# Optimization experiments

Hardware: AMD Instinct MI355X
Metric: run time of the kernel (lower is better)

The kernel has to match this reference:

```python
import jax, jax.numpy as jnp
import numpy as np
import math

B, S, D, H = 2, 2048, 1024, 16
DK = D // H


def setup_inputs() -> dict:
    key = jax.random.key(0)
    ks = jax.random.split(key, 8)
    s = 1.0 / math.sqrt(D)
    inp = {
        "query": jax.random.normal(ks[0], (B, S, D), jnp.float32),
        "key": jax.random.normal(ks[1], (B, S, D), jnp.float32),
        "value": jax.random.normal(ks[2], (B, S, D), jnp.float32),
        # causal mask: (1, 1, S, S), 1 where attention allowed
        "mask": jnp.tril(jnp.ones((S, S), jnp.int32))[None, None, :, :],
        "Wq": jax.random.normal(ks[3], (D, D), jnp.float32) * s,
        "Wk": jax.random.normal(ks[4], (D, D), jnp.float32) * s,
        "Wv": jax.random.normal(ks[5], (D, D), jnp.float32) * s,
        "Wo": jax.random.normal(ks[6], (D, D), jnp.float32) * s,
    }
    return inp


def reference(query, key, value, mask, Wq, Wk, Wv, Wo):
    # nn.Linear(bias=False): y = x @ W.T
    def proj_heads(x, W):
        y = jnp.einsum("bsd,ed->bse", x, W)          # (B,S,D)
        return y.reshape(B, -1, H, DK).transpose(0, 2, 1, 3)  # (B,H,S,DK)

    q = proj_heads(query, Wq)
    k = proj_heads(key, Wk)
    v = proj_heads(value, Wv)

    scale = jnp.asarray(math.sqrt(DK), q.dtype)
    scores = jnp.einsum("bhqd,bhkd->bhqk", q, k) / scale  # (B,H,S,S)
    scores = jnp.where(mask == 0, -jnp.inf, scores)
    attn = jax.nn.softmax(scores, axis=-1)
    # dropout p=0.0 (eval): identity
    out = jnp.einsum("bhqk,bhkd->bhqd", attn, v)          # (B,H,S,DK)
    concat = out.transpose(0, 2, 1, 3).reshape(B, -1, D)  # (B,S,D)
    return jnp.einsum("bsd,ed->bse", concat, Wo)
```

## Files before the change

### kernel.cpp

```cpp
#include <hip/hip_runtime.h>
#include <hip/hip_bf16.h>

#define B_ 2
#define S_ 2048
#define D_ 1024
#define H_ 16
#define DK_ 64

typedef __hip_bfloat16 bf16;
typedef __attribute__((ext_vector_type(8))) short bf16x8;
typedef __attribute__((ext_vector_type(4))) short bf16x4;
typedef __attribute__((ext_vector_type(4))) float f32x4;

#define GLDS16(g, l)                                                     \
    __builtin_amdgcn_global_load_lds(                                    \
        (const __attribute__((address_space(1))) void*)(g),              \
        (__attribute__((address_space(3))) void*)(l), 16, 0, 0)

#define MFMA_K32(a, b, c) __builtin_amdgcn_mfma_f32_16x16x32_bf16(a, b, c, 0, 0, 0)
#define MFMA_K16(a, b, c) __builtin_amdgcn_mfma_f32_16x16x16bf16_1k(a, b, c, 0, 0, 0)
#define EXP2F(x) __builtin_amdgcn_exp2f(x)

__global__ __launch_bounds__(256) void cvt_all(
    const float* __restrict__ q, const float* __restrict__ k, const float* __restrict__ v,
    const float* __restrict__ w0, const float* __restrict__ w1,
    const float* __restrict__ w2, const float* __restrict__ w3,
    bf16* __restrict__ oq, bf16* __restrict__ ok, bf16* __restrict__ ov,
    bf16* __restrict__ o0, bf16* __restrict__ o1, bf16* __restrict__ o2,
    bf16* __restrict__ o3) {
    int bid = blockIdx.x;
    const float* src; bf16* dst; int base;
    if      (bid < 2048) { src = q;  dst = oq; base = bid; }
    else if (bid < 4096) { src = k;  dst = ok; base = bid - 2048; }
    else if (bid < 6144) { src = v;  dst = ov; base = bid - 4096; }
    else if (bid < 6656) { src = w0; dst = o0; base = bid - 6144; }
    else if (bid < 7168) { src = w1; dst = o1; base = bid - 6656; }
    else if (bid < 7680) { src = w2; dst = o2; base = bid - 7168; }
    else                 { src = w3; dst = o3; base = bid - 7680; }
    int i = (base * 256 + threadIdx.x) * 8;
    float4 a = *(const float4*)(src + i);
    float4 b = *(const float4*)(src + i + 4);
    __align__(16) bf16 o[8];
    o[0] = __float2bfloat16(a.x); o[1] = __float2bfloat16(a.y);
    o[2] = __float2bfloat16(a.z); o[3] = __float2bfloat16(a.w);
    o[4] = __float2bfloat16(b.x); o[5] = __float2bfloat16(b.y);
    o[6] = __float2bfloat16(b.z); o[7] = __float2bfloat16(b.w);
    *(bf16x8*)(dst + i) = *(const bf16x8*)o;
}

template <int NT>
__device__ __forceinline__ void proj_loop(const bf16* __restrict__ X,
                                          const bf16* __restrict__ W,
                                          int m0, int n0, bf16* As, bf16* Bs,
                                          f32x4 (&acc)[2][NT]) {
    const int K = D_;
    const int tid = threadIdx.x;
    const int lane = tid & 63, wave = tid >> 6;
    const int lm = lane & 15, quad = lane >> 4;
    constexpr int BROWS = NT * 16;

    auto stage = [&](int t, int bf) {
        int k0 = t * 32;
        bf16* Ab = As + bf * (128 * 32);
        bf16* Bb = Bs + bf * (BROWS * 32);
#pragma unroll
        for (int i = 0; i < 2; ++i) {
            int s = i * 256 + tid;
            int row = s >> 2;
            int c = (s & 3) ^ ((row >> 1) & 3);
            GLDS16(X + (size_t)(m0 + row) * K + k0 + c * 8, Ab + s * 8);
        }
#pragma unroll
        for (int i = 0; i < NT / 4; ++i) {
            int s = i * 256 + tid;
            int row = s >> 2;
            int c = (s & 3) ^ ((row >> 1) & 3);
            GLDS16(W + (size_t)(n0 + row) * K + k0 + c * 8, Bb + s * 8);
        }
    };

    stage(0, 0);
    for (int t = 0; t < K / 32; ++t) {
        __syncthreads();
        if (t + 1 < K / 32) stage(t + 1, (t + 1) & 1);
        const bf16* Ab = As + (t & 1) * (128 * 32);
        const bf16* Bb = Bs + (t & 1) * (BROWS * 32);
        bf16x8 aF[2], bF[NT];
#pragma unroll
        for (int mt = 0; mt < 2; ++mt) {
            int row = wave * 32 + mt * 16 + lm;
            aF[mt] = *(const bf16x8*)(Ab + row * 32 + (quad ^ ((row >> 1) & 3)) * 8);
        }
#pragma unroll
        for (int nt = 0; nt < NT; ++nt) {
            int row = nt * 16 + lm;
            bF[nt] = *(const bf16x8*)(Bb + row * 32 + (quad ^ ((row >> 1) & 3)) * 8);
        }
#pragma unroll
        for (int mt = 0; mt < 2; ++mt)
#pragma unroll
            for (int nt = 0; nt < NT; ++nt)
                acc[mt][nt] = MFMA_K32(aF[mt], bF[nt], acc[mt][nt]);
    }
}

__global__ __launch_bounds__(256) void proj_qkv(
    const bf16* __restrict__ qx, const bf16* __restrict__ kx, const bf16* __restrict__ vx,
    const bf16* __restrict__ wq, const bf16* __restrict__ wk, const bf16* __restrict__ wv,
    bf16* __restrict__ qb, bf16* __restrict__ kb, bf16* __restrict__ vtb) {
    __shared__ __align__(16) bf16 As[2 * 128 * 32];
    __shared__ __align__(16) bf16 Bs[2 * 128 * 32];
    const int z = blockIdx.z;
    const bf16* X = (z == 0) ? qx : (z == 1) ? kx : vx;
    const bf16* W = (z == 0) ? wq : (z == 1) ? wk : wv;
    const int n0 = blockIdx.x * 128;
    const int m0 = blockIdx.y * 128;
    f32x4 acc[2][8] = {};
    proj_loop<8>(X, W, m0, n0, As, Bs, acc);

    const int lane = threadIdx.x & 63, wave = threadIdx.x >> 6;
    const int lm = lane & 15, quad = lane >> 4;
#pragma unroll
    for (int mt = 0; mt < 2; ++mt) {
        int mbase = m0 + wave * 32 + mt * 16 + quad * 4;
#pragma unroll
        for (int nt = 0; nt < 8; ++nt) {
            int n = n0 + nt * 16 + lm;
            if (z == 2) {
                int b = mbase >> 11, s = mbase & (S_ - 1);
                unsigned short u[4];
#pragma unroll
                for (int r = 0; r < 4; ++r) {
                    bf16 hv = __float2bfloat16(acc[mt][nt][r]);
                    u[r] = *(unsigned short*)&hv;
                }
                ushort4 pk = {u[0], u[1], u[2], u[3]};
                *(ushort4*)(vtb + ((size_t)(b * 1024 + n) * S_ + s)) = pk;
            } else {
                bf16* Y = z ? kb : qb;
#pragma unroll
                for (int r = 0; r < 4; ++r)
                    Y[(size_t)(mbase + r) * D_ + n] = __float2bfloat16(acc[mt][nt][r]);
            }
        }
    }
}

__global__ __launch_bounds__(256) void proj_o(const bf16* __restrict__ X,
                                              const bf16* __restrict__ W,
                                              float* __restrict__ Y) {
    __shared__ __align__(16) bf16 As[2 * 128 * 32];
    __shared__ __align__(16) bf16 Bs[2 * 64 * 32];
    const int n0 = blockIdx.x * 64;
    const int m0 = blockIdx.y * 128;
    f32x4 acc[2][4] = {};
    proj_loop<4>(X, W, m0, n0, As, Bs, acc);

    const int lane = threadIdx.x & 63, wave = threadIdx.x >> 6;
    const int lm = lane & 15, quad = lane >> 4;
#pragma unroll
    for (int mt = 0; mt < 2; ++mt) {
        int mbase = m0 + wave * 32 + mt * 16 + quad * 4;
#pragma unroll
        for (int nt = 0; nt < 4; ++nt) {
            int n = n0 + nt * 16 + lm;
#pragma unroll
            for (int r = 0; r < 4; ++r)
                Y[(size_t)(mbase + r) * D_ + n] = acc[mt][nt][r];
        }
    }
}

__global__ __launch_bounds__(512, 8) void attn_kernel(const bf16* __restrict__ Q,
                                                      const bf16* __restrict__ Kb,
                                                      const bf16* __restrict__ VT,
                                                      bf16* __restrict__ O) {
    __shared__ __align__(16) bf16 kt[2][64 * 64];
    __shared__ __align__(16) bf16 vt[2][64 * 64];

    const int tid = threadIdx.x;
    const int lane = tid & 63, wave = tid >> 6;
    const int g = wave & 3, half = wave >> 2;
    const int lm = lane & 15, quad = lane >> 4;
    const int qi = (int)(gridDim.x - 1 - blockIdx.x);
    const int h = blockIdx.y, b = blockIdx.z;
    const int q0 = qi * 64 + g * 16;

    const size_t bhoff = (size_t)b * S_ * D_ + (size_t)h * DK_;
    const bf16* vtb = VT + ((size_t)b * 1024 + h * DK_) * S_;

    const bf16* qp = Q + bhoff + (size_t)(q0 + lm) * D_ + quad * 8;
    bf16x8 aq0 = *(const bf16x8*)(qp);
    bf16x8 aq1 = *(const bf16x8*)(qp + 32);

    f32x4 oacc[4] = {};
    float lsum = 0.f;
    const float cexp = 0.125f * 1.44269504f;

    auto stage = [&](int i, int bf) {
        int j0s = i * 64;
        {
            int j = tid >> 3, c = (tid & 7) ^ (j & 7);
            GLDS16(Kb + bhoff + (size_t)(j0s + j) * D_ + c * 8, kt[bf] + tid * 8);
        }
        {
            int d = tid >> 3, c = (tid & 7) ^ (d & 7);
            GLDS16(vtb + (size_t)d * S_ + j0s + c * 8, vt[bf] + tid * 8);
        }
    };

    auto chunk = [&](const bf16* ktb, const bf16* vtl, int st, bool mk) {
        int j = st * 16 + lm;
        bf16x8 bk0 = *(const bf16x8*)(ktb + (((j << 3) | (quad ^ (j & 7))) * 8));
        bf16x8 bk1 = *(const bf16x8*)(ktb + (((j << 3) | ((4 + quad) ^ (j & 7))) * 8));
        f32x4 z = {};
        z = MFMA_K32(bk0, aq0, z);
        z = MFMA_K32(bk1, aq1, z);
        bf16x4 pa;
        float rs = 0.f;
#pragma unroll
        for (int r = 0; r < 4; ++r) {
            float p = EXP2F(z[r] * cexp);
            if (mk && (quad * 4 + r > lm)) p = 0.f;
            rs += p;
            bf16 hv = __float2bfloat16(p);
            pa[r] = *(short*)&hv;
        }
        lsum += rs;
#pragma unroll
        for (int dt = 0; dt < 4; ++dt) {
            int d = dt * 16 + lm;
            int cl = st * 2 + (quad >> 1);
            bf16x4 bv = *(const bf16x4*)(vtl + d * 64 +
                                         ((cl ^ (d & 7)) * 8 + (quad & 1) * 4));
            oacc[dt] = MFMA_K16(pa, bv, oacc[dt]);
        }
    };

    stage(0, 0);

    for (int i = 0; i <= qi; ++i) {
        __syncthreads();
        if (i < qi) stage(i + 1, (i + 1) & 1);
        const bf16* ktb = kt[i & 1];
        const bf16* vtl = vt[i & 1];
        if (i < qi) {
            chunk(ktb, vtl, 2 * half, false);
            chunk(ktb, vtl, 2 * half + 1, false);
        } else {
#pragma unroll
            for (int sti = 0; sti < 2; ++sti) {
                int st = 2 * half + sti;
                if (st < g) chunk(ktb, vtl, st, false);
                else if (st == g) chunk(ktb, vtl, st, true);
            }
        }
    }

    __syncthreads();
    float l = lsum;
    l += __shfl_xor(l, 16, 64);
    l += __shfl_xor(l, 32, 64);

    float* scro = (float*)kt;
    float* scrl = (float*)vt;
    if (half == 1) {
#pragma unroll
        for (int dt = 0; dt < 4; ++dt)
#pragma unroll
            for (int r = 0; r < 4; ++r)
                scro[((g * 4 + dt) * 4 + r) * 64 + lane] = oacc[dt][r];
        if (quad == 0) scrl[g * 16 + lm] = l;
    }
    __syncthreads();
    if (half == 0) {
        l += scrl[g * 16 + lm];
#pragma unroll
        for (int dt = 0; dt < 4; ++dt)
#pragma unroll
            for (int r = 0; r < 4; ++r)
                oacc[dt][r] += scro[((g * 4 + dt) * 4 + r) * 64 + lane];
#pragma unroll
        for (int r = 0; r < 4; ++r) {
            float inv = 1.f / __shfl(l, quad * 4 + r, 64);
            int qrow = q0 + quad * 4 + r;
#pragma unroll
            for (int dt = 0; dt < 4; ++dt) {
                int d = dt * 16 + lm;
                O[bhoff + (size_t)qrow * D_ + d] = __float2bfloat16(oacc[dt][r] * inv);
            }
        }
    }
}

extern "C" void kernel_launch(void* const* d_in, const int* in_sizes, int n_in,
                              void* d_out, int out_size, void* d_ws, size_t ws_size,
                              hipStream_t stream) {
    const float* q_in = (const float*)d_in[0];
    const float* k_in = (const float*)d_in[1];
    const float* v_in = (const float*)d_in[2];
    const float* Wq_f = (const float*)d_in[4];
    const float* Wk_f = (const float*)d_in[5];
    const float* Wv_f = (const float*)d_in[6];
    const float* Wo_f = (const float*)d_in[7];
    float* out = (float*)d_out;

    const size_t NEL = (size_t)B_ * S_ * D_;
    const size_t WEL = (size_t)D_ * D_;
    bf16* p = (bf16*)d_ws;
    bf16* qx = p;  p += NEL;
    bf16* kx = p;  p += NEL;
    bf16* vx = p;  p += NEL;
    bf16* wq = p;  p += WEL;
    bf16* wk = p;  p += WEL;
    bf16* wv = p;  p += WEL;
    bf16* wo = p;  p += WEL;
    bf16* qb = p;  p += NEL;
    bf16* kb = p;  p += NEL;
    bf16* vtb = p; p += NEL;
    bf16* cb = p;  p += NEL;

    cvt_all<<<8192, 256, 0, stream>>>(q_in, k_in, v_in, Wq_f, Wk_f, Wv_f, Wo_f,
                                      qx, kx, vx, wq, wk, wv, wo);

    dim3 gqkv(D_ / 128, (B_ * S_) / 128, 3);
    proj_qkv<<<gqkv, 256, 0, stream>>>(qx, kx, vx, wq, wk, wv, qb, kb, vtb);

    dim3 gattn(S_ / 64, H_, B_);
    attn_kernel<<<gattn, 512, 0, stream>>>(qb, kb, vtb, cb);

    dim3 gproj(D_ / 64, (B_ * S_) / 128);
    proj_o<<<gproj, 256, 0, stream>>>(cb, wo, out);
}
```

Baseline: 249.4 us.

## Enlarge attention tiles to 128 rows/keys and move V transpose to separate kernel

The attention kernel now processes 128 query rows per block with 16 waves (1024 threads) and stages 128-key K/V tiles, doubling reuse of each staged K/V tile and halving the number of blocks and iterations. The V projection epilogue no longer writes transposed scattered 8-byte stores; instead V is written row-major and a dedicated shared-memory transpose kernel produces V^T. This adds an extra launch and a full read/write of V, and the larger blocks raise LDS use and may lower occupancy and worsen causal load balance.

```diff
diff --git a/kernel.cpp b/kernel.cpp
--- a/kernel.cpp
+++ b/kernel.cpp
@@ -107,12 +107,13 @@
 __global__ __launch_bounds__(256) void proj_qkv(
     const bf16* __restrict__ qx, const bf16* __restrict__ kx, const bf16* __restrict__ vx,
     const bf16* __restrict__ wq, const bf16* __restrict__ wk, const bf16* __restrict__ wv,
-    bf16* __restrict__ qb, bf16* __restrict__ kb, bf16* __restrict__ vtb) {
+    bf16* __restrict__ qb, bf16* __restrict__ kb, bf16* __restrict__ vb) {
     __shared__ __align__(16) bf16 As[2 * 128 * 32];
     __shared__ __align__(16) bf16 Bs[2 * 128 * 32];
     const int z = blockIdx.z;
     const bf16* X = (z == 0) ? qx : (z == 1) ? kx : vx;
     const bf16* W = (z == 0) ? wq : (z == 1) ? wk : wv;
+    bf16* Y = (z == 0) ? qb : (z == 1) ? kb : vb;
     const int n0 = blockIdx.x * 128;
     const int m0 = blockIdx.y * 128;
     f32x4 acc[2][8] = {};
@@ -126,23 +127,34 @@
 #pragma unroll
         for (int nt = 0; nt < 8; ++nt) {
             int n = n0 + nt * 16 + lm;
-            if (z == 2) {
-                int b = mbase >> 11, s = mbase & (S_ - 1);
-                unsigned short u[4];
-#pragma unroll
-                for (int r = 0; r < 4; ++r) {
-                    bf16 hv = __float2bfloat16(acc[mt][nt][r]);
-                    u[r] = *(unsigned short*)&hv;
-                }
-                ushort4 pk = {u[0], u[1], u[2], u[3]};
-                *(ushort4*)(vtb + ((size_t)(b * 1024 + n) * S_ + s)) = pk;
-            } else {
-                bf16* Y = z ? kb : qb;
-#pragma unroll
-                for (int r = 0; r < 4; ++r)
-                    Y[(size_t)(mbase + r) * D_ + n] = __float2bfloat16(acc[mt][nt][r]);
-            }
-        }
+#pragma unroll
+            for (int r = 0; r < 4; ++r)
+                Y[(size_t)(mbase + r) * D_ + n] = __float2bfloat16(acc[mt][nt][r]);
+        }
+    }
+}
+
+__global__ __launch_bounds__(256) void transpose_v(const bf16* __restrict__ vb,
+                                                   bf16* __restrict__ vtb) {
+    __shared__ bf16 t[64][72];
+    const int s0 = blockIdx.x * 64, d0 = blockIdx.y * 64, b = blockIdx.z;
+    const int tid = threadIdx.x;
+    const int r = tid >> 3, c = tid & 7;
+    const bf16* src = vb + ((size_t)b * S_ + s0) * D_ + d0;
+#pragma unroll
+    for (int i = 0; i < 2; ++i) {
+        int s = r + i * 32;
+        *(bf16x8*)&t[s][c * 8] = *(const bf16x8*)(src + (size_t)s * D_ + c * 8);
+    }
+    __syncthreads();
+    bf16* dst = vtb + ((size_t)b * D_ + d0) * S_ + s0;
+#pragma unroll
+    for (int i = 0; i < 2; ++i) {
+        int d = r + i * 32;
+        __align__(16) bf16 o[8];
+#pragma unroll
+        for (int e = 0; e < 8; ++e) o[e] = t[c * 8 + e][d];
+        *(bf16x8*)(dst + (size_t)d * S_ + c * 8) = *(const bf16x8*)o;
     }
 }
 
@@ -171,20 +183,20 @@
     }
 }
 
-__global__ __launch_bounds__(512, 8) void attn_kernel(const bf16* __restrict__ Q,
-                                                      const bf16* __restrict__ Kb,
-                                                      const bf16* __restrict__ VT,
-                                                      bf16* __restrict__ O) {
-    __shared__ __align__(16) bf16 kt[2][64 * 64];
-    __shared__ __align__(16) bf16 vt[2][64 * 64];
+__global__ __launch_bounds__(1024, 8) void attn_kernel(const bf16* __restrict__ Q,
+                                                       const bf16* __restrict__ Kb,
+                                                       const bf16* __restrict__ VT,
+                                                       bf16* __restrict__ O) {
+    __shared__ __align__(16) bf16 kt[2][128 * 64];
+    __shared__ __align__(16) bf16 vt[2][64 * 128];
 
     const int tid = threadIdx.x;
     const int lane = tid & 63, wave = tid >> 6;
-    const int g = wave & 3, half = wave >> 2;
+    const int g = wave & 7, half = wave >> 3;
     const int lm = lane & 15, quad = lane >> 4;
     const int qi = (int)(gridDim.x - 1 - blockIdx.x);
     const int h = blockIdx.y, b = blockIdx.z;
-    const int q0 = qi * 64 + g * 16;
+    const int q0 = qi * 128 + g * 16;
 
     const size_t bhoff = (size_t)b * S_ * D_ + (size_t)h * DK_;
     const bf16* vtb = VT + ((size_t)b * 1024 + h * DK_) * S_;
@@ -198,13 +210,13 @@
     const float cexp = 0.125f * 1.44269504f;
 
     auto stage = [&](int i, int bf) {
-        int j0s = i * 64;
+        int j0s = i * 128;
         {
             int j = tid >> 3, c = (tid & 7) ^ (j & 7);
             GLDS16(Kb + bhoff + (size_t)(j0s + j) * D_ + c * 8, kt[bf] + tid * 8);
         }
         {
-            int d = tid >> 3, c = (tid & 7) ^ (d & 7);
+            int d = tid >> 4, c = (tid & 15) ^ (d & 15);
             GLDS16(vtb + (size_t)d * S_ + j0s + c * 8, vt[bf] + tid * 8);
         }
     };
@@ -231,8 +243,8 @@
         for (int dt = 0; dt < 4; ++dt) {
             int d = dt * 16 + lm;
             int cl = st * 2 + (quad >> 1);
-            bf16x4 bv = *(const bf16x4*)(vtl + d * 64 +
-                                         ((cl ^ (d & 7)) * 8 + (quad & 1) * 4));
+            bf16x4 bv = *(const bf16x4*)(vtl + d * 128 +
+                                         ((cl ^ (d & 15)) * 8 + (quad & 1) * 4));
             oacc[dt] = MFMA_K16(pa, bv, oacc[dt]);
         }
     };
@@ -245,12 +257,12 @@
         const bf16* ktb = kt[i & 1];
         const bf16* vtl = vt[i & 1];
         if (i < qi) {
-            chunk(ktb, vtl, 2 * half, false);
-            chunk(ktb, vtl, 2 * half + 1, false);
+#pragma unroll
+            for (int sti = 0; sti < 4; ++sti) chunk(ktb, vtl, half * 4 + sti, false);
         } else {
 #pragma unroll
-            for (int sti = 0; sti < 2; ++sti) {
-                int st = 2 * half + sti;
+            for (int sti = 0; sti < 4; ++sti) {
+                int st = half * 4 + sti;
                 if (st < g) chunk(ktb, vtl, st, false);
                 else if (st == g) chunk(ktb, vtl, st, true);
             }
@@ -317,6 +329,7 @@
     bf16* wo = p;  p += WEL;
     bf16* qb = p;  p += NEL;
     bf16* kb = p;  p += NEL;
+    bf16* vb = p;  p += NEL;
     bf16* vtb = p; p += NEL;
     bf16* cb = p;  p += NEL;
 
@@ -324,10 +337,13 @@
                                       qx, kx, vx, wq, wk, wv, wo);
 
     dim3 gqkv(D_ / 128, (B_ * S_) / 128, 3);
-    proj_qkv<<<gqkv, 256, 0, stream>>>(qx, kx, vx, wq, wk, wv, qb, kb, vtb);
-
-    dim3 gattn(S_ / 64, H_, B_);
-    attn_kernel<<<gattn, 512, 0, stream>>>(qb, kb, vtb, cb);
+    proj_qkv<<<gqkv, 256, 0, stream>>>(qx, kx, vx, wq, wk, wv, qb, kb, vb);
+
+    dim3 gtr(S_ / 64, D_ / 64, B_);
+    transpose_v<<<gtr, 256, 0, stream>>>(vb, vtb);
+
+    dim3 gattn(S_ / 128, H_, B_);
+    attn_kernel<<<gattn, 1024, 0, stream>>>(qb, kb, vtb, cb);
 
     dim3 gproj(D_ / 64, (B_ * S_) / 128);
     proj_o<<<gproj, 256, 0, stream>>>(cb, wo, out);
```

Measured after the change: 265.3 us. +6.4%, slower.
